# Performance work log

Hardware: AMD Instinct MI355X
Metric: run time of the kernel (lower is better)

The kernel has to match this reference:

```python
import jax, jax.numpy as jnp
import numpy as np

NSTEP, NGRID, MU = 730, 2000, 16
PRECS = 1e-5

# HBV parameter scaling ranges (parascaLst)
_LO = np.array([1, 50, 0.05, 0.01, 0.001, 0.2, 0, 0, -2.5, 0.5, 0, 0, 0.3], dtype=np.float32)
_HI = np.array([6, 1000, 0.9, 0.5, 0.2, 1, 10, 100, 2.5, 10, 0.1, 0.2, 5], dtype=np.float32)


def setup_inputs() -> dict:
    key = jax.random.key(0)
    k1, k2 = jax.random.split(key)
    u = jax.random.uniform(k1, (NSTEP, NGRID, 3), dtype=jnp.float32)
    # channel 0: precip [0,10]; channel 1: temp [-5,15]; channel 2: PET [0,5]
    scale = jnp.array([10.0, 20.0, 5.0], dtype=jnp.float32)
    shift = jnp.array([0.0, -5.0, 0.0], dtype=jnp.float32)
    x = u * scale + shift
    parameters = jax.random.uniform(k2, (NGRID, 13, MU), dtype=jnp.float32)
    return {"x": x, "parameters": parameters, "mu": MU}


def _hbv_forward(x, parameters, mu):
    Ngrid = x.shape[1]
    lo = jnp.asarray(_LO)[None, :, None]
    hi = jnp.asarray(_HI)[None, :, None]
    p = lo + parameters * (hi - lo)  # [Ngrid, 13, mu]
    (parBETA, parFC, parK0, parK1, parK2, parLP, parPERC, parUZL,
     parTT, parCFMAX, parCFR, parCWH, parBETAET) = [p[:, i, :] for i in range(13)]

    init = jnp.full((Ngrid, mu), 0.001, dtype=jnp.float32)
    state0 = (init, init, init, init, init)  # SNOWPACK, MELTWATER, SM, SUZ, SLZ

    def step(carry, inp):
        SP, MW, SM, SUZ, SLZ = carry
        Pt, Tt, Et = inp  # each [Ngrid]
        Pt, Tt, Et = Pt[:, None], Tt[:, None], Et[:, None]  # broadcast over mu
        rain = Pt * (Tt >= parTT).astype(jnp.float32)
        snow = Pt * (Tt < parTT).astype(jnp.float32)
        SP = SP + snow
        melt = jnp.minimum(jnp.maximum(parCFMAX * (Tt - parTT), 0.0), SP)
        MW = MW + melt
        SP = SP - melt
        refreezing = jnp.minimum(jnp.maximum(parCFR * parCFMAX * (parTT - Tt), 0.0), MW)
        SP = SP + refreezing
        MW = MW - refreezing
        tosoil = jnp.maximum(MW - parCWH * SP, 0.0)
        MW = MW - tosoil
        soil_wetness = jnp.clip((SM / parFC) ** parBETA, 0.0, 1.0)
        recharge = (rain + tosoil) * soil_wetness
        SM = SM + rain + tosoil - recharge
        excess = jnp.maximum(SM - parFC, 0.0)
        SM = SM - excess
        evapfactor = jnp.clip((SM / (parLP * parFC)) ** parBETAET, 0.0, 1.0)
        ETact = jnp.minimum(SM, Et * evapfactor)
        SM = jnp.maximum(SM - ETact, PRECS)
        SUZ = SUZ + recharge + excess
        PERC = jnp.minimum(SUZ, parPERC)
        SUZ = SUZ - PERC
        Q0 = parK0 * jnp.maximum(SUZ - parUZL, 0.0)
        SUZ = SUZ - Q0
        Q1 = parK1 * SUZ
        SUZ = SUZ - Q1
        SLZ = SLZ + PERC
        Q2 = parK2 * SLZ
        SLZ = SLZ - Q2
        return (SP, MW, SM, SUZ, SLZ), Q0 + Q1 + Q2

    xs = (x[:, :, 0], x[:, :, 1], x[:, :, 2])
    _, Qsimmu = jax.lax.scan(step, state0, xs)  # [Nstep, Ngrid, mu]
    Qsimave = Qsimmu.mean(-1)  # muwts=None -> mean over components
    return Qsimave[..., None]  # [Nstep, Ngrid, 1]  (routOpt=False)


def reference(x, parameters, mu):
    return _hbv_forward(x, parameters, mu)
```

## Files before the change

kernel.cpp:

```cpp
#include <hip/hip_runtime.h>

#define NSTEP  730
#define NGRID  2000
#define PRECSf 1e-5f

#define GLOBAL_AS __attribute__((address_space(1)))
#define LDS_AS    __attribute__((address_space(3)))

__device__ __forceinline__ float fast_exp2(float v) { return __builtin_amdgcn_exp2f(v); }
__device__ __forceinline__ float fast_log2(float v) { return __builtin_amdgcn_logf(v); }
__device__ __forceinline__ float med3(float a, float b, float c) {
    return __builtin_amdgcn_fmed3f(a, b, c);
}

struct Par {
    float TT, cfmax, cfmaxTT, cfrXcf, cfrTT, CWH;
    float beta, betaC, FC, betaet, betaetC;
    float PERC, omK0, k0uzl, omK1, K2;
};

#define MEMFENCE() asm volatile("" ::: "memory")
#define WAITV(N)  asm volatile("s_waitcnt vmcnt(" #N ")" ::: "memory")

template<int I>
__device__ __forceinline__ void snow1(const float4 (&xv)[16],
        float& SP, float& MW,
        float (&A)[16], float (&Ets)[16], float (&cEts)[16], const Par& c)
{
    const float Pt = xv[I].x, Tt = xv[I].y, Ex = xv[I].z;

    const float snow = (Tt < c.TT) ? Pt : 0.0f;
    const float rain = Pt - snow;
    const float mraw = fmaf(c.cfmax,   Tt, -c.cfmaxTT);
    const float rraw = fmaf(-c.cfrXcf, Tt,  c.cfrTT );
    const float SP1  = SP + snow;
    const float SP2  = med3(SP1 - mraw, 0.0f, SP1);
    const float MW1  = MW + (SP1 - SP2);
    const float MW2  = med3(MW1 - rraw, 0.0f, MW1);
    SP = SP2 + (MW1 - MW2);
    const float tosoil = fmaxf(fmaf(-c.CWH, SP, MW2), 0.0f);
    MW = MW2 - tosoil;
    A[I]    = rain + tosoil;
    Ets[I]  = Ex;
    cEts[I] = c.betaetC + fast_log2(Ex);
}

template<int I>
__device__ __forceinline__ void soil1(const float (&A)[16], const float (&Ets)[16],
        const float (&cEts)[16], float (&qbuf)[16],
        float& SM, float& SUZ, float& SLZ, const Par& c)
{
    const float Ac  = A[I];
    const float Et  = Ets[I];
    const float cEt = cEts[I];

    const float SMpA = SM + Ac;
    const float sw   = fast_exp2(fmaf(c.beta, fast_log2(SM), c.betaC));
    const float SM1  = fmaf(-Ac, sw, SMpA);
    const float SM2  = fminf(SM1, c.FC);
    const float inflow = SMpA - SM2;
    const float Ete  = fast_exp2(fmaf(c.betaet, fast_log2(SM2), cEt));
    SM = fmaxf(fmaxf(SM2 - Ete, SM2 - Et), PRECSf);

    const float SUZ1  = SUZ + inflow;
    const float PERCv = fminf(SUZ1, c.PERC);
    const float SUZ2  = SUZ1 - PERCv;
    const float SUZ3  = fminf(SUZ2, fmaf(c.omK0, SUZ2, c.k0uzl));
    const float SUZ4  = c.omK1 * SUZ3;
    SUZ = SUZ4;
    const float SLZ1 = SLZ + PERCv;
    const float Q2   = c.K2 * SLZ1;
    SLZ = SLZ1 - Q2;

    qbuf[I] = (SUZ2 - SUZ4) + Q2;
}

template<int I, int NS>
__device__ __forceinline__ void snow_pass(const float4 (&xv)[16],
        float& SP, float& MW, float (&A)[16], float (&Ets)[16], float (&cEts)[16],
        const Par& c)
{
    if constexpr (I < NS) {
        snow1<I>(xv, SP, MW, A, Ets, cEts, c);
        snow_pass<I + 1, NS>(xv, SP, MW, A, Ets, cEts, c);
    }
}

template<int I, int NS>
__device__ __forceinline__ void soil_pass(const float (&A)[16], const float (&Ets)[16],
        const float (&cEts)[16], float (&qbuf)[16],
        float& SM, float& SUZ, float& SLZ, const Par& c)
{
    if constexpr (I < NS) {
        soil1<I>(A, Ets, cEts, qbuf, SM, SUZ, SLZ, c);
        soil_pass<I + 1, NS>(A, Ets, cEts, qbuf, SM, SUZ, SLZ, c);
    }
}

template<int I, int NS>
__device__ __forceinline__ void both_pass(const float4 (&xv)[16],
        float& SP, float& MW,
        float (&An)[16], float (&Etn)[16], float (&cEtn)[16],
        const float (&Ac)[16], const float (&Etc)[16], const float (&cEtc)[16],
        float (&qbuf)[16],
        float& SM, float& SUZ, float& SLZ, const Par& c)
{
    if constexpr (I < NS) {
        soil1<I>(Ac, Etc, cEtc, qbuf, SM, SUZ, SLZ, c);
        snow1<I>(xv, SP, MW, An, Etn, cEtn, c);
        both_pass<I + 1, NS>(xv, SP, MW, An, Etn, cEtn, Ac, Etc, cEtc,
                             qbuf, SM, SUZ, SLZ, c);
    }
}

#define LOAD_XV(B)                                                             \
    _Pragma("unroll")                                                          \
    for (int i = 0; i < 16; ++i)                                               \
        xv[i] = *reinterpret_cast<const float4*>(&xs[B][i * 16 + crow * 4]);   \
    asm volatile("" :: "v"(xv[0].x),  "v"(xv[1].x),  "v"(xv[2].x),             \
                       "v"(xv[3].x),  "v"(xv[4].x),  "v"(xv[5].x),             \
                       "v"(xv[6].x),  "v"(xv[7].x),  "v"(xv[8].x),             \
                       "v"(xv[9].x),  "v"(xv[10].x), "v"(xv[11].x),            \
                       "v"(xv[12].x), "v"(xv[13].x), "v"(xv[14].x),            \
                       "v"(xv[15].x))

#define REDUCE_STORE(T0, N) do {                                               \
    float* qrow = &qt[crow * 336 + m * 20];                                    \
    *reinterpret_cast<float4*>(qrow + 0)  = make_float4(qbuf[0], qbuf[1], qbuf[2], qbuf[3]);   \
    *reinterpret_cast<float4*>(qrow + 4)  = make_float4(qbuf[4], qbuf[5], qbuf[6], qbuf[7]);   \
    *reinterpret_cast<float4*>(qrow + 8)  = make_float4(qbuf[8], qbuf[9], qbuf[10], qbuf[11]); \
    *reinterpret_cast<float4*>(qrow + 12) = make_float4(qbuf[12], qbuf[13], qbuf[14], qbuf[15]);\
    const float* qcol = &qt[crow * 336 + m];                                   \
    float s0 = qcol[0*20]  + qcol[1*20];                                       \
    float s1 = qcol[2*20]  + qcol[3*20];                                       \
    float s2 = qcol[4*20]  + qcol[5*20];                                       \
    float s3 = qcol[6*20]  + qcol[7*20];                                       \
    float s4 = qcol[8*20]  + qcol[9*20];                                       \
    float s5 = qcol[10*20] + qcol[11*20];                                      \
    float s6 = qcol[12*20] + qcol[13*20];                                      \
    float s7 = qcol[14*20] + qcol[15*20];                                      \
    s0 += s1; s2 += s3; s4 += s5; s6 += s7;                                    \
    s0 += s2; s4 += s6;                                                        \
    s0 += s4;                                                                  \
    if (m < (N)) out[(size_t)((T0) + m) * NGRID + g] = s0 * 0.0625f;           \
} while (0)

__global__ __launch_bounds__(64, 1)
void hbv_kernel(const float* __restrict__ x,
                const float* __restrict__ params,
                float* __restrict__ out)
{
    __shared__ __align__(16) float xs[2][256];
    __shared__ __align__(16) float qt[4 * 336];

    const int lane = threadIdx.x;
    const int g0   = blockIdx.x * 4;
    const int crow = lane >> 4;
    const int m    = lane & 15;
    const int g    = g0 + crow;

    const float* srcb[4];
    int ioff[4];
#pragma unroll
    for (int j = 0; j < 4; ++j) {
        const int flat = j * 64 + lane;
        const int i    = flat >> 4;
        const int cc   = (flat >> 2) & 3;
        int comp       = flat & 3; if (comp == 3) comp = 0;
        srcb[j] = x + (size_t)(g0 + cc) * 3 + comp;
        ioff[j] = i;
    }

#define ISSUE(B, T0) do {                                                      \
    MEMFENCE();                                                                \
    _Pragma("unroll")                                                          \
    for (int j = 0; j < 4; ++j) {                                              \
        int stp = (T0) + ioff[j]; stp = stp < NSTEP ? stp : NSTEP - 1;         \
        const float* s_ = srcb[j] + (size_t)stp * (NGRID * 3);                 \
        __builtin_amdgcn_global_load_lds((const GLOBAL_AS unsigned*)s_,        \
            (LDS_AS unsigned*)&xs[B][j * 64], 4, 0, 0);                        \
    }                                                                          \
    MEMFENCE();                                                                \
} while (0)

    const float lo[13] = {1.f,50.f,0.05f,0.01f,0.001f,0.2f,0.f,0.f,-2.5f,0.5f,0.f,0.f,0.3f};
    const float hi[13] = {6.f,1000.f,0.9f,0.5f,0.2f,1.f,10.f,100.f,2.5f,10.f,0.1f,0.2f,5.f};
    float p[13];
    const float* pg = params + ((size_t)g * 13) * 16 + m;
#pragma unroll
    for (int i = 0; i < 13; ++i) p[i] = lo[i] + pg[(size_t)i * 16] * (hi[i] - lo[i]);

    Par c;
    c.TT      = p[8];
    c.cfmax   = p[9];
    c.cfmaxTT = p[9] * p[8];
    c.cfrXcf  = p[10] * p[9];
    c.cfrTT   = c.cfrXcf * p[8];
    c.CWH     = p[11];
    c.beta    = p[0];
    c.betaC   = -p[0] * fast_log2(p[1]);
    c.FC      = p[1];
    c.betaet  = p[12];
    c.betaetC = -p[12] * fast_log2(p[5] * p[1]);
    c.PERC    = p[6];
    c.omK0    = 1.0f - p[2];
    c.k0uzl   = p[2] * p[7];
    c.omK1    = 1.0f - p[3];
    c.K2      = p[4];

    float SP = 0.001f, MW = 0.001f, SM = 0.001f, SUZ = 0.001f, SLZ = 0.001f;

    float4 xv[16];
    float Aa[16], EtA[16], cEtA[16];
    float Ab[16], EtB[16], cEtB[16];
    float qbuf[16];

    ISSUE(0, 0);
    ISSUE(1, 16);
    WAITV(4);
    LOAD_XV(0);
    snow_pass<0, 16>(xv, SP, MW, Aa, EtA, cEtA, c);

#define BODY_W(K, WN, AC_, ETC_, CETC_, AN_, ETN_, CETN_)                      \
    WAITV(WN);                                                                 \
    LOAD_XV(((K) + 1) & 1);                                                    \
    ISSUE((K) & 1, ((K) + 2) * 16);                                            \
    both_pass<0, 16>(xv, SP, MW, AN_, ETN_, CETN_, AC_, ETC_, CETC_,           \
                     qbuf, SM, SUZ, SLZ, c);                                   \
    REDUCE_STORE((K) * 16, 16);

    BODY_W(0, 0, Aa, EtA, cEtA, Ab, EtB, cEtB);

    for (int kk = 0; kk < 22; ++kk) {
        const int k0 = 1 + kk * 2;
        BODY_W(k0,     20, Ab, EtB, cEtB, Aa, EtA, cEtA);
        BODY_W(k0 + 1, 20, Aa, EtA, cEtA, Ab, EtB, cEtB);
    }
#undef BODY_W

    soil_pass<0, 10>(Ab, EtB, cEtB, qbuf, SM, SUZ, SLZ, c);
    REDUCE_STORE(720, 10);
#undef ISSUE
}

extern "C" void kernel_launch(void* const* d_in, const int* in_sizes, int n_in,
                              void* d_out, int out_size, void* d_ws, size_t ws_size,
                              hipStream_t stream)
{
    const float* x      = (const float*)d_in[0];
    const float* params = (const float*)d_in[1];
    float* out          = (float*)d_out;

    hipLaunchKernelGGL(hbv_kernel, dim3(500), dim3(64), 0, stream, x, params, out);
}
```

Before: 83.80 us.

## Split snow and soil recurrences across two wavefronts with LDS handoff

The single-wave kernel becomes a two-wave producer/consumer pipeline. Wave 0 loads inputs and runs the snow recurrence for the next 16-step chunk, then writes the intermediates to a double-buffered LDS array. Wave 1 runs the soil/groundwater recurrence on the previous chunk and writes per-step discharge to LDS, which wave 0 reduces and stores. The aim is to run the two serial dependency chains in parallel on separate waves, at the cost of a block barrier per chunk and extra LDS traffic. The evapotranspiration term now uses the log of SM1 instead of the clamped SM2, which changes the math whenever SM1 exceeds FC.

```diff
diff --git a/kernel.cpp b/kernel.cpp
--- a/kernel.cpp
+++ b/kernel.cpp
@@ -20,7 +20,10 @@
 };
 
 #define MEMFENCE() asm volatile("" ::: "memory")
-#define WAITV(N)  asm volatile("s_waitcnt vmcnt(" #N ")" ::: "memory")
+#define WAITV(N)   asm volatile("s_waitcnt vmcnt(" #N ")" ::: "memory")
+#define BAR() do { MEMFENCE();                                                 \
+    asm volatile("s_waitcnt lgkmcnt(0)" ::: "memory");                         \
+    __builtin_amdgcn_s_barrier(); MEMFENCE(); } while (0)
 
 template<int I>
 __device__ __forceinline__ void snow1(const float4 (&xv)[16],
@@ -59,7 +62,7 @@
     const float SM1  = fmaf(-Ac, sw, SMpA);
     const float SM2  = fminf(SM1, c.FC);
     const float inflow = SMpA - SM2;
-    const float Ete  = fast_exp2(fmaf(c.betaet, fast_log2(SM2), cEt));
+    const float Ete  = fast_exp2(fmaf(c.betaet, fast_log2(SM1), cEt));
     SM = fmaxf(fmaxf(SM2 - Ete, SM2 - Et), PRECSf);
 
     const float SUZ1  = SUZ + inflow;
@@ -97,26 +100,10 @@
     }
 }
 
-template<int I, int NS>
-__device__ __forceinline__ void both_pass(const float4 (&xv)[16],
-        float& SP, float& MW,
-        float (&An)[16], float (&Etn)[16], float (&cEtn)[16],
-        const float (&Ac)[16], const float (&Etc)[16], const float (&cEtc)[16],
-        float (&qbuf)[16],
-        float& SM, float& SUZ, float& SLZ, const Par& c)
-{
-    if constexpr (I < NS) {
-        soil1<I>(Ac, Etc, cEtc, qbuf, SM, SUZ, SLZ, c);
-        snow1<I>(xv, SP, MW, An, Etn, cEtn, c);
-        both_pass<I + 1, NS>(xv, SP, MW, An, Etn, cEtn, Ac, Etc, cEtc,
-                             qbuf, SM, SUZ, SLZ, c);
-    }
-}
-
 #define LOAD_XV(B)                                                             \
     _Pragma("unroll")                                                          \
-    for (int i = 0; i < 16; ++i)                                               \
-        xv[i] = *reinterpret_cast<const float4*>(&xs[B][i * 16 + crow * 4]);   \
+    for (int ii = 0; ii < 16; ++ii)                                            \
+        xv[ii] = *reinterpret_cast<const float4*>(&xs[B][ii * 16 + crow * 4]); \
     asm volatile("" :: "v"(xv[0].x),  "v"(xv[1].x),  "v"(xv[2].x),             \
                        "v"(xv[3].x),  "v"(xv[4].x),  "v"(xv[5].x),             \
                        "v"(xv[6].x),  "v"(xv[7].x),  "v"(xv[8].x),             \
@@ -124,13 +111,37 @@
                        "v"(xv[12].x), "v"(xv[13].x), "v"(xv[14].x),            \
                        "v"(xv[15].x))
 
-#define REDUCE_STORE(T0, N) do {                                               \
-    float* qrow = &qt[crow * 336 + m * 20];                                    \
-    *reinterpret_cast<float4*>(qrow + 0)  = make_float4(qbuf[0], qbuf[1], qbuf[2], qbuf[3]);   \
-    *reinterpret_cast<float4*>(qrow + 4)  = make_float4(qbuf[4], qbuf[5], qbuf[6], qbuf[7]);   \
-    *reinterpret_cast<float4*>(qrow + 8)  = make_float4(qbuf[8], qbuf[9], qbuf[10], qbuf[11]); \
+#define AB_WRITE(BUF)                                                          \
+    _Pragma("unroll")                                                          \
+    for (int q = 0; q < 4; ++q) {                                              \
+        ab[BUF][q    ][lane] = make_float4(A[4*q],   A[4*q+1],   A[4*q+2],   A[4*q+3]);    \
+        ab[BUF][4 + q][lane] = make_float4(Ets[4*q], Ets[4*q+1], Ets[4*q+2], Ets[4*q+3]);  \
+        ab[BUF][8 + q][lane] = make_float4(cEts[4*q],cEts[4*q+1],cEts[4*q+2],cEts[4*q+3]); \
+    }
+
+#define AB_READ(BUF) do {                                                      \
+    _Pragma("unroll")                                                          \
+    for (int j = 0; j < 12; ++j) rr[j] = ab[BUF][j][lane];                     \
+    asm volatile("" :: "v"(rr[0].x), "v"(rr[1].x), "v"(rr[2].x), "v"(rr[3].x), \
+                       "v"(rr[4].x), "v"(rr[5].x), "v"(rr[6].x), "v"(rr[7].x), \
+                       "v"(rr[8].x), "v"(rr[9].x), "v"(rr[10].x),"v"(rr[11].x));\
+    const float* rf = reinterpret_cast<const float*>(rr);                      \
+    _Pragma("unroll")                                                          \
+    for (int kk = 0; kk < 16; ++kk) {                                          \
+        Ac[kk] = rf[kk]; Etc[kk] = rf[16 + kk]; cEtc[kk] = rf[32 + kk];        \
+    }                                                                          \
+} while (0)
+
+#define QT_WRITE(BUF) do {                                                     \
+    float* qrow = &qt[BUF][crow * 336 + m * 20];                               \
+    *reinterpret_cast<float4*>(qrow + 0)  = make_float4(qbuf[0], qbuf[1], qbuf[2], qbuf[3]);    \
+    *reinterpret_cast<float4*>(qrow + 4)  = make_float4(qbuf[4], qbuf[5], qbuf[6], qbuf[7]);    \
+    *reinterpret_cast<float4*>(qrow + 8)  = make_float4(qbuf[8], qbuf[9], qbuf[10], qbuf[11]);  \
     *reinterpret_cast<float4*>(qrow + 12) = make_float4(qbuf[12], qbuf[13], qbuf[14], qbuf[15]);\
-    const float* qcol = &qt[crow * 336 + m];                                   \
+} while (0)
+
+#define REDUCE_OUT(BUF, T0, N) do {                                            \
+    const float* qcol = &qt[BUF][crow * 336 + m];                              \
     float s0 = qcol[0*20]  + qcol[1*20];                                       \
     float s1 = qcol[2*20]  + qcol[3*20];                                       \
     float s2 = qcol[4*20]  + qcol[5*20];                                       \
@@ -140,20 +151,22 @@
     float s6 = qcol[12*20] + qcol[13*20];                                      \
     float s7 = qcol[14*20] + qcol[15*20];                                      \
     s0 += s1; s2 += s3; s4 += s5; s6 += s7;                                    \
-    s0 += s2; s4 += s6;                                                        \
-    s0 += s4;                                                                  \
+    s0 += s2; s4 += s6; s0 += s4;                                              \
     if (m < (N)) out[(size_t)((T0) + m) * NGRID + g] = s0 * 0.0625f;           \
 } while (0)
 
-__global__ __launch_bounds__(64, 1)
+__global__ __launch_bounds__(128, 1)
 void hbv_kernel(const float* __restrict__ x,
                 const float* __restrict__ params,
                 float* __restrict__ out)
 {
-    __shared__ __align__(16) float xs[2][256];
-    __shared__ __align__(16) float qt[4 * 336];
-
-    const int lane = threadIdx.x;
+    __shared__ __align__(16) float4 ab[2][12][64];
+    __shared__ __align__(16) float  xs[2][256];
+    __shared__ __align__(16) float  qt[2][4 * 336];
+
+    const int tid  = threadIdx.x;
+    const int wid  = tid >> 6;
+    const int lane = tid & 63;
     const int g0   = blockIdx.x * 4;
     const int crow = lane >> 4;
     const int m    = lane & 15;
@@ -211,35 +224,42 @@
     float SP = 0.001f, MW = 0.001f, SM = 0.001f, SUZ = 0.001f, SLZ = 0.001f;
 
     float4 xv[16];
-    float Aa[16], EtA[16], cEtA[16];
-    float Ab[16], EtB[16], cEtB[16];
-    float qbuf[16];
-
-    ISSUE(0, 0);
-    ISSUE(1, 16);
-    WAITV(4);
-    LOAD_XV(0);
-    snow_pass<0, 16>(xv, SP, MW, Aa, EtA, cEtA, c);
-
-#define BODY_W(K, WN, AC_, ETC_, CETC_, AN_, ETN_, CETN_)                      \
-    WAITV(WN);                                                                 \
-    LOAD_XV(((K) + 1) & 1);                                                    \
-    ISSUE((K) & 1, ((K) + 2) * 16);                                            \
-    both_pass<0, 16>(xv, SP, MW, AN_, ETN_, CETN_, AC_, ETC_, CETC_,           \
-                     qbuf, SM, SUZ, SLZ, c);                                   \
-    REDUCE_STORE((K) * 16, 16);
-
-    BODY_W(0, 0, Aa, EtA, cEtA, Ab, EtB, cEtB);
-
-    for (int kk = 0; kk < 22; ++kk) {
-        const int k0 = 1 + kk * 2;
-        BODY_W(k0,     20, Ab, EtB, cEtB, Aa, EtA, cEtA);
-        BODY_W(k0 + 1, 20, Aa, EtA, cEtA, Ab, EtB, cEtB);
-    }
-#undef BODY_W
-
-    soil_pass<0, 10>(Ab, EtB, cEtB, qbuf, SM, SUZ, SLZ, c);
-    REDUCE_STORE(720, 10);
+    float  A[16], Ets[16], cEts[16];
+    float4 rr[12];
+    float  Ac[16], Etc[16], cEtc[16];
+    float  qbuf[16];
+
+    if (wid == 0) {
+        ISSUE(0, 0);
+        ISSUE(1, 16);
+        WAITV(4);
+        LOAD_XV(0);
+        snow_pass<0, 16>(xv, SP, MW, A, Ets, cEts, c);
+        AB_WRITE(0);
+    }
+    BAR();
+
+    for (int i = 0; i < 46; ++i) {
+        if (wid == 0) {
+            if (i <= 43) ISSUE(i & 1, (i + 2) * 16);
+            if (i <= 44) {
+                if (i == 44)      { WAITV(16); }
+                else if (i >= 2)  { WAITV(20); }
+                else              { WAITV(4);  }
+                LOAD_XV((i + 1) & 1);
+                snow_pass<0, 16>(xv, SP, MW, A, Ets, cEts, c);
+                AB_WRITE((i + 1) & 1);
+            }
+            if (i >= 1) REDUCE_OUT((i - 1) & 1, (i - 1) * 16, 16);
+        } else {
+            AB_READ(i & 1);
+            if (i < 45) soil_pass<0, 16>(Ac, Etc, cEtc, qbuf, SM, SUZ, SLZ, c);
+            else        soil_pass<0, 10>(Ac, Etc, cEtc, qbuf, SM, SUZ, SLZ, c);
+            QT_WRITE(i & 1);
+        }
+        BAR();
+    }
+    if (wid == 0) REDUCE_OUT(1, 720, 10);
 #undef ISSUE
 }
 
@@ -251,5 +271,5 @@
     const float* params = (const float*)d_in[1];
     float* out          = (float*)d_out;
 
-    hipLaunchKernelGGL(hbv_kernel, dim3(500), dim3(64), 0, stream, x, params, out);
-}
+    hipLaunchKernelGGL(hbv_kernel, dim3(500), dim3(128), 0, stream, x, params, out);
+}
```

Measured after the change: 91.77 us. 9.5% more time.

## Process two mu components per lane and eight grid cells per wavefront

Applied to the files above, without the earlier changes.

Each lane now carries two independent HBV state chains (mu j and j+8), so a wavefront covers eight grid cells and the launch halves to 250 blocks. The two interleaved recurrences give the scheduler independent work to hide the latency of the serial per-step dependency chain. The staging buffers, load issue pattern and LDS reduction are resized for the new mapping, and the evapotranspiration power now uses SM1 instead of the clamped SM2, which can change results when soil moisture exceeds FC. Fewer wavefronts run than there are compute units, and register pressure roughly doubles.

```diff
diff --git a/kernel.cpp b/kernel.cpp
--- a/kernel.cpp
+++ b/kernel.cpp
@@ -22,13 +22,9 @@
 #define MEMFENCE() asm volatile("" ::: "memory")
 #define WAITV(N)  asm volatile("s_waitcnt vmcnt(" #N ")" ::: "memory")
 
-template<int I>
-__device__ __forceinline__ void snow1(const float4 (&xv)[16],
-        float& SP, float& MW,
-        float (&A)[16], float (&Ets)[16], float (&cEts)[16], const Par& c)
-{
-    const float Pt = xv[I].x, Tt = xv[I].y, Ex = xv[I].z;
-
+__device__ __forceinline__ float snow_core(float Pt, float Tt,
+        float& SP, float& MW, const Par& c)
+{
     const float snow = (Tt < c.TT) ? Pt : 0.0f;
     const float rain = Pt - snow;
     const float mraw = fmaf(c.cfmax,   Tt, -c.cfmaxTT);
@@ -40,26 +36,18 @@
     SP = SP2 + (MW1 - MW2);
     const float tosoil = fmaxf(fmaf(-c.CWH, SP, MW2), 0.0f);
     MW = MW2 - tosoil;
-    A[I]    = rain + tosoil;
-    Ets[I]  = Ex;
-    cEts[I] = c.betaetC + fast_log2(Ex);
-}
-
-template<int I>
-__device__ __forceinline__ void soil1(const float (&A)[16], const float (&Ets)[16],
-        const float (&cEts)[16], float (&qbuf)[16],
+    return rain + tosoil;
+}
+
+__device__ __forceinline__ float soil_core(float Ac, float Et, float cEt,
         float& SM, float& SUZ, float& SLZ, const Par& c)
 {
-    const float Ac  = A[I];
-    const float Et  = Ets[I];
-    const float cEt = cEts[I];
-
     const float SMpA = SM + Ac;
     const float sw   = fast_exp2(fmaf(c.beta, fast_log2(SM), c.betaC));
     const float SM1  = fmaf(-Ac, sw, SMpA);
     const float SM2  = fminf(SM1, c.FC);
     const float inflow = SMpA - SM2;
-    const float Ete  = fast_exp2(fmaf(c.betaet, fast_log2(SM2), cEt));
+    const float Ete  = fast_exp2(fmaf(c.betaet, fast_log2(SM1), cEt));
     SM = fmaxf(fmaxf(SM2 - Ete, SM2 - Et), PRECSf);
 
     const float SUZ1  = SUZ + inflow;
@@ -71,52 +59,90 @@
     const float SLZ1 = SLZ + PERCv;
     const float Q2   = c.K2 * SLZ1;
     SLZ = SLZ1 - Q2;
-
-    qbuf[I] = (SUZ2 - SUZ4) + Q2;
+    return (SUZ2 - SUZ4) + Q2;
+}
+
+template<int I>
+__device__ __forceinline__ void snow1(const float4 (&xv)[16],
+        float& SP0, float& MW0, float& SP1, float& MW1,
+        float (&A0)[16], float (&A1)[16], float (&Ets)[16],
+        float (&cE0)[16], float (&cE1)[16],
+        const Par& c0, const Par& c1)
+{
+    const float Pt = xv[I].x, Tt = xv[I].y, Ex = xv[I].z;
+    const float lEx = fast_log2(Ex);
+    Ets[I] = Ex;
+    A0[I] = snow_core(Pt, Tt, SP0, MW0, c0);
+    cE0[I] = c0.betaetC + lEx;
+    A1[I] = snow_core(Pt, Tt, SP1, MW1, c1);
+    cE1[I] = c1.betaetC + lEx;
+}
+
+template<int I>
+__device__ __forceinline__ void soil1(const float (&A0)[16], const float (&A1)[16],
+        const float (&Ets)[16], const float (&cE0)[16], const float (&cE1)[16],
+        float (&qbuf)[16],
+        float& SM0, float& SUZ0, float& SLZ0,
+        float& SM1, float& SUZ1, float& SLZ1,
+        const Par& c0, const Par& c1)
+{
+    const float q0 = soil_core(A0[I], Ets[I], cE0[I], SM0, SUZ0, SLZ0, c0);
+    const float q1 = soil_core(A1[I], Ets[I], cE1[I], SM1, SUZ1, SLZ1, c1);
+    qbuf[I] = q0 + q1;
 }
 
 template<int I, int NS>
 __device__ __forceinline__ void snow_pass(const float4 (&xv)[16],
-        float& SP, float& MW, float (&A)[16], float (&Ets)[16], float (&cEts)[16],
-        const Par& c)
+        float& SP0, float& MW0, float& SP1, float& MW1,
+        float (&A0)[16], float (&A1)[16], float (&Ets)[16],
+        float (&cE0)[16], float (&cE1)[16], const Par& c0, const Par& c1)
 {
     if constexpr (I < NS) {
-        snow1<I>(xv, SP, MW, A, Ets, cEts, c);
-        snow_pass<I + 1, NS>(xv, SP, MW, A, Ets, cEts, c);
+        snow1<I>(xv, SP0, MW0, SP1, MW1, A0, A1, Ets, cE0, cE1, c0, c1);
+        snow_pass<I + 1, NS>(xv, SP0, MW0, SP1, MW1, A0, A1, Ets, cE0, cE1, c0, c1);
     }
 }
 
 template<int I, int NS>
-__device__ __forceinline__ void soil_pass(const float (&A)[16], const float (&Ets)[16],
-        const float (&cEts)[16], float (&qbuf)[16],
-        float& SM, float& SUZ, float& SLZ, const Par& c)
+__device__ __forceinline__ void soil_pass(const float (&A0)[16], const float (&A1)[16],
+        const float (&Ets)[16], const float (&cE0)[16], const float (&cE1)[16],
+        float (&qbuf)[16],
+        float& SM0, float& SUZ0, float& SLZ0,
+        float& SM1, float& SUZ1, float& SLZ1,
+        const Par& c0, const Par& c1)
 {
     if constexpr (I < NS) {
-        soil1<I>(A, Ets, cEts, qbuf, SM, SUZ, SLZ, c);
-        soil_pass<I + 1, NS>(A, Ets, cEts, qbuf, SM, SUZ, SLZ, c);
+        soil1<I>(A0, A1, Ets, cE0, cE1, qbuf, SM0, SUZ0, SLZ0, SM1, SUZ1, SLZ1, c0, c1);
+        soil_pass<I + 1, NS>(A0, A1, Ets, cE0, cE1, qbuf,
+                             SM0, SUZ0, SLZ0, SM1, SUZ1, SLZ1, c0, c1);
     }
 }
 
 template<int I, int NS>
 __device__ __forceinline__ void both_pass(const float4 (&xv)[16],
-        float& SP, float& MW,
-        float (&An)[16], float (&Etn)[16], float (&cEtn)[16],
-        const float (&Ac)[16], const float (&Etc)[16], const float (&cEtc)[16],
+        float& SP0, float& MW0, float& SP1, float& MW1,
+        float (&An0)[16], float (&An1)[16], float (&Etn)[16],
+        float (&cEn0)[16], float (&cEn1)[16],
+        const float (&Ac0)[16], const float (&Ac1)[16], const float (&Etc)[16],
+        const float (&cEc0)[16], const float (&cEc1)[16],
         float (&qbuf)[16],
-        float& SM, float& SUZ, float& SLZ, const Par& c)
+        float& SM0, float& SUZ0, float& SLZ0,
+        float& SM1, float& SUZ1, float& SLZ1,
+        const Par& c0, const Par& c1)
 {
     if constexpr (I < NS) {
-        soil1<I>(Ac, Etc, cEtc, qbuf, SM, SUZ, SLZ, c);
-        snow1<I>(xv, SP, MW, An, Etn, cEtn, c);
-        both_pass<I + 1, NS>(xv, SP, MW, An, Etn, cEtn, Ac, Etc, cEtc,
-                             qbuf, SM, SUZ, SLZ, c);
+        soil1<I>(Ac0, Ac1, Etc, cEc0, cEc1, qbuf, SM0, SUZ0, SLZ0, SM1, SUZ1, SLZ1, c0, c1);
+        snow1<I>(xv, SP0, MW0, SP1, MW1, An0, An1, Etn, cEn0, cEn1, c0, c1);
+        both_pass<I + 1, NS>(xv, SP0, MW0, SP1, MW1, An0, An1, Etn, cEn0, cEn1,
+                             Ac0, Ac1, Etc, cEc0, cEc1, qbuf,
+                             SM0, SUZ0, SLZ0, SM1, SUZ1, SLZ1, c0, c1);
     }
 }
 
 #define LOAD_XV(B)                                                             \
     _Pragma("unroll")                                                          \
-    for (int i = 0; i < 16; ++i)                                               \
-        xv[i] = *reinterpret_cast<const float4*>(&xs[B][i * 16 + crow * 4]);   \
+    for (int ii = 0; ii < 16; ++ii)                                            \
+        xv[ii] = *reinterpret_cast<const float4*>(&xs[B][ii * 32 + cc * 4]);   \
     asm volatile("" :: "v"(xv[0].x),  "v"(xv[1].x),  "v"(xv[2].x),             \
                        "v"(xv[3].x),  "v"(xv[4].x),  "v"(xv[5].x),             \
                        "v"(xv[6].x),  "v"(xv[7].x),  "v"(xv[8].x),             \
@@ -125,24 +151,25 @@
                        "v"(xv[15].x))
 
 #define REDUCE_STORE(T0, N) do {                                               \
-    float* qrow = &qt[crow * 336 + m * 20];                                    \
-    *reinterpret_cast<float4*>(qrow + 0)  = make_float4(qbuf[0], qbuf[1], qbuf[2], qbuf[3]);   \
-    *reinterpret_cast<float4*>(qrow + 4)  = make_float4(qbuf[4], qbuf[5], qbuf[6], qbuf[7]);   \
-    *reinterpret_cast<float4*>(qrow + 8)  = make_float4(qbuf[8], qbuf[9], qbuf[10], qbuf[11]); \
+    float* qrow = &qt[cc * 168 + j2 * 20];                                     \
+    *reinterpret_cast<float4*>(qrow + 0)  = make_float4(qbuf[0], qbuf[1], qbuf[2], qbuf[3]);    \
+    *reinterpret_cast<float4*>(qrow + 4)  = make_float4(qbuf[4], qbuf[5], qbuf[6], qbuf[7]);    \
+    *reinterpret_cast<float4*>(qrow + 8)  = make_float4(qbuf[8], qbuf[9], qbuf[10], qbuf[11]);  \
     *reinterpret_cast<float4*>(qrow + 12) = make_float4(qbuf[12], qbuf[13], qbuf[14], qbuf[15]);\
-    const float* qcol = &qt[crow * 336 + m];                                   \
-    float s0 = qcol[0*20]  + qcol[1*20];                                       \
-    float s1 = qcol[2*20]  + qcol[3*20];                                       \
-    float s2 = qcol[4*20]  + qcol[5*20];                                       \
-    float s3 = qcol[6*20]  + qcol[7*20];                                       \
-    float s4 = qcol[8*20]  + qcol[9*20];                                       \
-    float s5 = qcol[10*20] + qcol[11*20];                                      \
-    float s6 = qcol[12*20] + qcol[13*20];                                      \
-    float s7 = qcol[14*20] + qcol[15*20];                                      \
-    s0 += s1; s2 += s3; s4 += s5; s6 += s7;                                    \
-    s0 += s2; s4 += s6;                                                        \
-    s0 += s4;                                                                  \
-    if (m < (N)) out[(size_t)((T0) + m) * NGRID + g] = s0 * 0.0625f;           \
+    const float* qc1 = &qt[cc * 168 + j2];                                     \
+    float a0 = qc1[0*20] + qc1[1*20];                                          \
+    float a1 = qc1[2*20] + qc1[3*20];                                          \
+    float a2 = qc1[4*20] + qc1[5*20];                                          \
+    float a3 = qc1[6*20] + qc1[7*20];                                          \
+    a0 += a1; a2 += a3; a0 += a2;                                              \
+    out[(size_t)((T0) + j2) * NGRID + g] = a0 * 0.0625f;                       \
+    const float* qc2 = &qt[cc * 168 + 8 + j2];                                 \
+    float b0 = qc2[0*20] + qc2[1*20];                                          \
+    float b1 = qc2[2*20] + qc2[3*20];                                          \
+    float b2 = qc2[4*20] + qc2[5*20];                                          \
+    float b3 = qc2[6*20] + qc2[7*20];                                          \
+    b0 += b1; b2 += b3; b0 += b2;                                              \
+    if (8 + j2 < (N)) out[(size_t)((T0) + 8 + j2) * NGRID + g] = b0 * 0.0625f; \
 } while (0)
 
 __global__ __launch_bounds__(64, 1)
@@ -150,31 +177,31 @@
                 const float* __restrict__ params,
                 float* __restrict__ out)
 {
-    __shared__ __align__(16) float xs[2][256];
-    __shared__ __align__(16) float qt[4 * 336];
+    __shared__ __align__(16) float xs[2][512];
+    __shared__ __align__(16) float qt[8 * 168];
 
     const int lane = threadIdx.x;
-    const int g0   = blockIdx.x * 4;
-    const int crow = lane >> 4;
-    const int m    = lane & 15;
-    const int g    = g0 + crow;
-
-    const float* srcb[4];
-    int ioff[4];
+    const int g0   = blockIdx.x * 8;
+    const int cc   = lane >> 3;
+    const int j2   = lane & 7;
+    const int g    = g0 + cc;
+
+    const float* srcb[8];
+    int ioff[8];
 #pragma unroll
-    for (int j = 0; j < 4; ++j) {
+    for (int j = 0; j < 8; ++j) {
         const int flat = j * 64 + lane;
-        const int i    = flat >> 4;
-        const int cc   = (flat >> 2) & 3;
+        const int i    = flat >> 5;
+        const int ce   = (flat >> 2) & 7;
         int comp       = flat & 3; if (comp == 3) comp = 0;
-        srcb[j] = x + (size_t)(g0 + cc) * 3 + comp;
+        srcb[j] = x + (size_t)(g0 + ce) * 3 + comp;
         ioff[j] = i;
     }
 
 #define ISSUE(B, T0) do {                                                      \
     MEMFENCE();                                                                \
     _Pragma("unroll")                                                          \
-    for (int j = 0; j < 4; ++j) {                                              \
+    for (int j = 0; j < 8; ++j) {                                              \
         int stp = (T0) + ioff[j]; stp = stp < NSTEP ? stp : NSTEP - 1;         \
         const float* s_ = srcb[j] + (size_t)stp * (NGRID * 3);                 \
         __builtin_amdgcn_global_load_lds((const GLOBAL_AS unsigned*)s_,        \
@@ -185,60 +212,71 @@
 
     const float lo[13] = {1.f,50.f,0.05f,0.01f,0.001f,0.2f,0.f,0.f,-2.5f,0.5f,0.f,0.f,0.3f};
     const float hi[13] = {6.f,1000.f,0.9f,0.5f,0.2f,1.f,10.f,100.f,2.5f,10.f,0.1f,0.2f,5.f};
-    float p[13];
-    const float* pg = params + ((size_t)g * 13) * 16 + m;
+    float p0[13], p1[13];
+    const float* pg = params + ((size_t)g * 13) * 16;
 #pragma unroll
-    for (int i = 0; i < 13; ++i) p[i] = lo[i] + pg[(size_t)i * 16] * (hi[i] - lo[i]);
-
-    Par c;
-    c.TT      = p[8];
-    c.cfmax   = p[9];
-    c.cfmaxTT = p[9] * p[8];
-    c.cfrXcf  = p[10] * p[9];
-    c.cfrTT   = c.cfrXcf * p[8];
-    c.CWH     = p[11];
-    c.beta    = p[0];
-    c.betaC   = -p[0] * fast_log2(p[1]);
-    c.FC      = p[1];
-    c.betaet  = p[12];
-    c.betaetC = -p[12] * fast_log2(p[5] * p[1]);
-    c.PERC    = p[6];
-    c.omK0    = 1.0f - p[2];
-    c.k0uzl   = p[2] * p[7];
-    c.omK1    = 1.0f - p[3];
+    for (int i = 0; i < 13; ++i) {
+        p0[i] = lo[i] + pg[(size_t)i * 16 + j2    ] * (hi[i] - lo[i]);
+        p1[i] = lo[i] + pg[(size_t)i * 16 + j2 + 8] * (hi[i] - lo[i]);
+    }
+
+#define MKPAR(c, p)                                                            \
+    c.TT      = p[8];                                                          \
+    c.cfmax   = p[9];                                                          \
+    c.cfmaxTT = p[9] * p[8];                                                   \
+    c.cfrXcf  = p[10] * p[9];                                                  \
+    c.cfrTT   = c.cfrXcf * p[8];                                               \
+    c.CWH     = p[11];                                                         \
+    c.beta    = p[0];                                                          \
+    c.betaC   = -p[0] * fast_log2(p[1]);                                       \
+    c.FC      = p[1];                                                          \
+    c.betaet  = p[12];                                                         \
+    c.betaetC = -p[12] * fast_log2(p[5] * p[1]);                               \
+    c.PERC    = p[6];                                                          \
+    c.omK0    = 1.0f - p[2];                                                   \
+    c.k0uzl   = p[2] * p[7];                                                   \
+    c.omK1    = 1.0f - p[3];                                                   \
     c.K2      = p[4];
 
-    float SP = 0.001f, MW = 0.001f, SM = 0.001f, SUZ = 0.001f, SLZ = 0.001f;
+    Par c0, c1;
+    MKPAR(c0, p0);
+    MKPAR(c1, p1);
+#undef MKPAR
+
+    float SP0 = 0.001f, MW0 = 0.001f, SM0 = 0.001f, SUZ0 = 0.001f, SLZ0 = 0.001f;
+    float SP1 = 0.001f, MW1 = 0.001f, SM1 = 0.001f, SUZ1 = 0.001f, SLZ1 = 0.001f;
 
     float4 xv[16];
-    float Aa[16], EtA[16], cEtA[16];
-    float Ab[16], EtB[16], cEtB[16];
+    float A0a[16], A1a[16], Eta[16], cE0a[16], cE1a[16];
+    float A0b[16], A1b[16], Etb[16], cE0b[16], cE1b[16];
     float qbuf[16];
 
     ISSUE(0, 0);
     ISSUE(1, 16);
-    WAITV(4);
+    WAITV(8);
     LOAD_XV(0);
-    snow_pass<0, 16>(xv, SP, MW, Aa, EtA, cEtA, c);
-
-#define BODY_W(K, WN, AC_, ETC_, CETC_, AN_, ETN_, CETN_)                      \
+    snow_pass<0, 16>(xv, SP0, MW0, SP1, MW1, A0a, A1a, Eta, cE0a, cE1a, c0, c1);
+
+#define BODY_W(K, WN, AC0,AC1,ETC,CEC0,CEC1, AN0,AN1,ETN,CEN0,CEN1)            \
     WAITV(WN);                                                                 \
     LOAD_XV(((K) + 1) & 1);                                                    \
     ISSUE((K) & 1, ((K) + 2) * 16);                                            \
-    both_pass<0, 16>(xv, SP, MW, AN_, ETN_, CETN_, AC_, ETC_, CETC_,           \
-                     qbuf, SM, SUZ, SLZ, c);                                   \
+    both_pass<0, 16>(xv, SP0, MW0, SP1, MW1, AN0, AN1, ETN, CEN0, CEN1,        \
+                     AC0, AC1, ETC, CEC0, CEC1, qbuf,                          \
+                     SM0, SUZ0, SLZ0, SM1, SUZ1, SLZ1, c0, c1);                \
     REDUCE_STORE((K) * 16, 16);
 
-    BODY_W(0, 0, Aa, EtA, cEtA, Ab, EtB, cEtB);
+    BODY_W(0, 0, A0a,A1a,Eta,cE0a,cE1a, A0b,A1b,Etb,cE0b,cE1b);
 
     for (int kk = 0; kk < 22; ++kk) {
         const int k0 = 1 + kk * 2;
-        BODY_W(k0,     20, Ab, EtB, cEtB, Aa, EtA, cEtA);
-        BODY_W(k0 + 1, 20, Aa, EtA, cEtA, Ab, EtB, cEtB);
+        BODY_W(k0,     2, A0b,A1b,Etb,cE0b,cE1b, A0a,A1a,Eta,cE0a,cE1a);
+        BODY_W(k0 + 1, 2, A0a,A1a,Eta,cE0a,cE1a, A0b,A1b,Etb,cE0b,cE1b);
     }
 #undef BODY_W
 
-    soil_pass<0, 10>(Ab, EtB, cEtB, qbuf, SM, SUZ, SLZ, c);
+    soil_pass<0, 10>(A0b, A1b, Etb, cE0b, cE1b, qbuf,
+                     SM0, SUZ0, SLZ0, SM1, SUZ1, SLZ1, c0, c1);
     REDUCE_STORE(720, 10);
 #undef ISSUE
 }
@@ -251,5 +289,5 @@
     const float* params = (const float*)d_in[1];
     float* out          = (float*)d_out;
 
-    hipLaunchKernelGGL(hbv_kernel, dim3(500), dim3(64), 0, stream, x, params, out);
-}
+    hipLaunchKernelGGL(hbv_kernel, dim3(250), dim3(64), 0, stream, x, params, out);
+}
```

Result: slower. 143.1 us (+70.8%).

## Software-pipeline routing one step behind soil update and drop precomputed log of PET

Applied to the files above, without the earlier changes.

Restructures the per-step recurrence so the groundwater routing of step I-1 is interleaved with the soil update of step I, which shortens the serial dependency chain through SM. It also interleaves the snow computation with the soil math. The evaporation term is now computed as Et*exp2(...) instead of adding log2(Et) inside the exponent, which removes one log per step and the cEt arrays. The vmcnt wait threshold changes from 20 to 16. The risks are slightly different rounding and higher register pressure from the extra live values.

```diff
diff --git a/kernel.cpp b/kernel.cpp
--- a/kernel.cpp
+++ b/kernel.cpp
@@ -22,47 +22,10 @@
 #define MEMFENCE() asm volatile("" ::: "memory")
 #define WAITV(N)  asm volatile("s_waitcnt vmcnt(" #N ")" ::: "memory")
 
-template<int I>
-__device__ __forceinline__ void snow1(const float4 (&xv)[16],
-        float& SP, float& MW,
-        float (&A)[16], float (&Ets)[16], float (&cEts)[16], const Par& c)
-{
-    const float Pt = xv[I].x, Tt = xv[I].y, Ex = xv[I].z;
-
-    const float snow = (Tt < c.TT) ? Pt : 0.0f;
-    const float rain = Pt - snow;
-    const float mraw = fmaf(c.cfmax,   Tt, -c.cfmaxTT);
-    const float rraw = fmaf(-c.cfrXcf, Tt,  c.cfrTT );
-    const float SP1  = SP + snow;
-    const float SP2  = med3(SP1 - mraw, 0.0f, SP1);
-    const float MW1  = MW + (SP1 - SP2);
-    const float MW2  = med3(MW1 - rraw, 0.0f, MW1);
-    SP = SP2 + (MW1 - MW2);
-    const float tosoil = fmaxf(fmaf(-c.CWH, SP, MW2), 0.0f);
-    MW = MW2 - tosoil;
-    A[I]    = rain + tosoil;
-    Ets[I]  = Ex;
-    cEts[I] = c.betaetC + fast_log2(Ex);
-}
-
-template<int I>
-__device__ __forceinline__ void soil1(const float (&A)[16], const float (&Ets)[16],
-        const float (&cEts)[16], float (&qbuf)[16],
-        float& SM, float& SUZ, float& SLZ, const Par& c)
-{
-    const float Ac  = A[I];
-    const float Et  = Ets[I];
-    const float cEt = cEts[I];
-
-    const float SMpA = SM + Ac;
-    const float sw   = fast_exp2(fmaf(c.beta, fast_log2(SM), c.betaC));
-    const float SM1  = fmaf(-Ac, sw, SMpA);
-    const float SM2  = fminf(SM1, c.FC);
-    const float inflow = SMpA - SM2;
-    const float Ete  = fast_exp2(fmaf(c.betaet, fast_log2(SM2), cEt));
-    SM = fmaxf(fmaxf(SM2 - Ete, SM2 - Et), PRECSf);
-
-    const float SUZ1  = SUZ + inflow;
+__device__ __forceinline__ float route_step(float infl,
+        float& SUZ, float& SLZ, const Par& c)
+{
+    const float SUZ1  = SUZ + infl;
     const float PERCv = fminf(SUZ1, c.PERC);
     const float SUZ2  = SUZ1 - PERCv;
     const float SUZ3  = fminf(SUZ2, fmaf(c.omK0, SUZ2, c.k0uzl));
@@ -71,52 +34,93 @@
     const float SLZ1 = SLZ + PERCv;
     const float Q2   = c.K2 * SLZ1;
     SLZ = SLZ1 - Q2;
-
-    qbuf[I] = (SUZ2 - SUZ4) + Q2;
+    return (SUZ2 - SUZ4) + Q2;
+}
+
+template<int I, bool SNOW>
+__device__ __forceinline__ void step1(const float4 (&xv)[16],
+        const float (&A)[16], const float (&Ets)[16],
+        float (&An)[16], float (&Etn)[16],
+        float (&qbuf)[16], float& infl,
+        float& SM, float& SUZ, float& SLZ,
+        float& SP, float& MW, const Par& c)
+{
+    const float Ac   = A[I];
+    const float Et   = Ets[I];
+    const float SMpA = SM + Ac;
+    const float lg   = fast_log2(SM);
+    float rain = 0.0f, SP2v = 0.0f, MW1v = 0.0f, rrawv = 0.0f, Ex = 0.0f;
+    if constexpr (SNOW) {
+        const float Pt = xv[I].x, Tt = xv[I].y;
+        Ex = xv[I].z;
+        const float snow = (Tt < c.TT) ? Pt : 0.0f;
+        rain = Pt - snow;
+        const float mraw = fmaf(c.cfmax, Tt, -c.cfmaxTT);
+        rrawv = fmaf(-c.cfrXcf, Tt, c.cfrTT);
+        const float SP1 = SP + snow;
+        SP2v = med3(SP1 - mraw, 0.0f, SP1);
+        MW1v = MW + (SP1 - SP2v);
+    }
+    const float sw = fast_exp2(fmaf(c.beta, lg, c.betaC));
+    if constexpr (I >= 1) qbuf[I - 1] = route_step(infl, SUZ, SLZ, c);
+    const float SM1 = fmaf(-Ac, sw, SMpA);
+    const float lg1 = fast_log2(SM1);
+    if constexpr (SNOW) {
+        const float MW2 = med3(MW1v - rrawv, 0.0f, MW1v);
+        SP = SP2v + (MW1v - MW2);
+        const float tosoil = fmaxf(fmaf(-c.CWH, SP, MW2), 0.0f);
+        MW = MW2 - tosoil;
+        An[I]  = rain + tosoil;
+        Etn[I] = Ex;
+    }
+    const float SM2 = fminf(SM1, c.FC);
+    infl = SMpA - SM2;
+    const float Ete = Et * fast_exp2(fmaf(c.betaet, lg1, c.betaetC));
+    SM = fmaxf(fmaxf(SM2 - Ete, SM2 - Et), PRECSf);
+}
+
+template<int I, int NS, bool SNOW>
+__device__ __forceinline__ void steps_pass(const float4 (&xv)[16],
+        const float (&A)[16], const float (&Ets)[16],
+        float (&An)[16], float (&Etn)[16],
+        float (&qbuf)[16], float& infl,
+        float& SM, float& SUZ, float& SLZ,
+        float& SP, float& MW, const Par& c)
+{
+    if constexpr (I < NS) {
+        step1<I, SNOW>(xv, A, Ets, An, Etn, qbuf, infl, SM, SUZ, SLZ, SP, MW, c);
+        steps_pass<I + 1, NS, SNOW>(xv, A, Ets, An, Etn, qbuf, infl,
+                                    SM, SUZ, SLZ, SP, MW, c);
+    }
 }
 
 template<int I, int NS>
 __device__ __forceinline__ void snow_pass(const float4 (&xv)[16],
-        float& SP, float& MW, float (&A)[16], float (&Ets)[16], float (&cEts)[16],
-        const Par& c)
+        float& SP, float& MW, float (&A)[16], float (&Ets)[16], const Par& c)
 {
     if constexpr (I < NS) {
-        snow1<I>(xv, SP, MW, A, Ets, cEts, c);
-        snow_pass<I + 1, NS>(xv, SP, MW, A, Ets, cEts, c);
-    }
-}
-
-template<int I, int NS>
-__device__ __forceinline__ void soil_pass(const float (&A)[16], const float (&Ets)[16],
-        const float (&cEts)[16], float (&qbuf)[16],
-        float& SM, float& SUZ, float& SLZ, const Par& c)
-{
-    if constexpr (I < NS) {
-        soil1<I>(A, Ets, cEts, qbuf, SM, SUZ, SLZ, c);
-        soil_pass<I + 1, NS>(A, Ets, cEts, qbuf, SM, SUZ, SLZ, c);
-    }
-}
-
-template<int I, int NS>
-__device__ __forceinline__ void both_pass(const float4 (&xv)[16],
-        float& SP, float& MW,
-        float (&An)[16], float (&Etn)[16], float (&cEtn)[16],
-        const float (&Ac)[16], const float (&Etc)[16], const float (&cEtc)[16],
-        float (&qbuf)[16],
-        float& SM, float& SUZ, float& SLZ, const Par& c)
-{
-    if constexpr (I < NS) {
-        soil1<I>(Ac, Etc, cEtc, qbuf, SM, SUZ, SLZ, c);
-        snow1<I>(xv, SP, MW, An, Etn, cEtn, c);
-        both_pass<I + 1, NS>(xv, SP, MW, An, Etn, cEtn, Ac, Etc, cEtc,
-                             qbuf, SM, SUZ, SLZ, c);
+        const float Pt = xv[I].x, Tt = xv[I].y, Ex = xv[I].z;
+        const float snow = (Tt < c.TT) ? Pt : 0.0f;
+        const float rain = Pt - snow;
+        const float mraw = fmaf(c.cfmax, Tt, -c.cfmaxTT);
+        const float rraw = fmaf(-c.cfrXcf, Tt, c.cfrTT);
+        const float SP1  = SP + snow;
+        const float SP2  = med3(SP1 - mraw, 0.0f, SP1);
+        const float MW1  = MW + (SP1 - SP2);
+        const float MW2  = med3(MW1 - rraw, 0.0f, MW1);
+        SP = SP2 + (MW1 - MW2);
+        const float tosoil = fmaxf(fmaf(-c.CWH, SP, MW2), 0.0f);
+        MW = MW2 - tosoil;
+        A[I]   = rain + tosoil;
+        Ets[I] = Ex;
+        snow_pass<I + 1, NS>(xv, SP, MW, A, Ets, c);
     }
 }
 
 #define LOAD_XV(B)                                                             \
     _Pragma("unroll")                                                          \
-    for (int i = 0; i < 16; ++i)                                               \
-        xv[i] = *reinterpret_cast<const float4*>(&xs[B][i * 16 + crow * 4]);   \
+    for (int ii = 0; ii < 16; ++ii)                                            \
+        xv[ii] = *reinterpret_cast<const float4*>(&xs[B][ii * 16 + crow * 4]); \
     asm volatile("" :: "v"(xv[0].x),  "v"(xv[1].x),  "v"(xv[2].x),             \
                        "v"(xv[3].x),  "v"(xv[4].x),  "v"(xv[5].x),             \
                        "v"(xv[6].x),  "v"(xv[7].x),  "v"(xv[8].x),             \
@@ -126,9 +130,9 @@
 
 #define REDUCE_STORE(T0, N) do {                                               \
     float* qrow = &qt[crow * 336 + m * 20];                                    \
-    *reinterpret_cast<float4*>(qrow + 0)  = make_float4(qbuf[0], qbuf[1], qbuf[2], qbuf[3]);   \
-    *reinterpret_cast<float4*>(qrow + 4)  = make_float4(qbuf[4], qbuf[5], qbuf[6], qbuf[7]);   \
-    *reinterpret_cast<float4*>(qrow + 8)  = make_float4(qbuf[8], qbuf[9], qbuf[10], qbuf[11]); \
+    *reinterpret_cast<float4*>(qrow + 0)  = make_float4(qbuf[0], qbuf[1], qbuf[2], qbuf[3]);    \
+    *reinterpret_cast<float4*>(qrow + 4)  = make_float4(qbuf[4], qbuf[5], qbuf[6], qbuf[7]);    \
+    *reinterpret_cast<float4*>(qrow + 8)  = make_float4(qbuf[8], qbuf[9], qbuf[10], qbuf[11]);  \
     *reinterpret_cast<float4*>(qrow + 12) = make_float4(qbuf[12], qbuf[13], qbuf[14], qbuf[15]);\
     const float* qcol = &qt[crow * 336 + m];                                   \
     float s0 = qcol[0*20]  + qcol[1*20];                                       \
@@ -140,8 +144,7 @@
     float s6 = qcol[12*20] + qcol[13*20];                                      \
     float s7 = qcol[14*20] + qcol[15*20];                                      \
     s0 += s1; s2 += s3; s4 += s5; s6 += s7;                                    \
-    s0 += s2; s4 += s6;                                                        \
-    s0 += s4;                                                                  \
+    s0 += s2; s4 += s6; s0 += s4;                                              \
     if (m < (N)) out[(size_t)((T0) + m) * NGRID + g] = s0 * 0.0625f;           \
 } while (0)
 
@@ -211,34 +214,38 @@
     float SP = 0.001f, MW = 0.001f, SM = 0.001f, SUZ = 0.001f, SLZ = 0.001f;
 
     float4 xv[16];
-    float Aa[16], EtA[16], cEtA[16];
-    float Ab[16], EtB[16], cEtB[16];
+    float Aa[16], Eta[16];
+    float Ab[16], Etb[16];
     float qbuf[16];
+    float infl = 0.0f;
 
     ISSUE(0, 0);
     ISSUE(1, 16);
     WAITV(4);
     LOAD_XV(0);
-    snow_pass<0, 16>(xv, SP, MW, Aa, EtA, cEtA, c);
-
-#define BODY_W(K, WN, AC_, ETC_, CETC_, AN_, ETN_, CETN_)                      \
+    snow_pass<0, 16>(xv, SP, MW, Aa, Eta, c);
+
+#define BODY_W(K, WN, AC_, ETC_, AN_, ETN_)                                    \
     WAITV(WN);                                                                 \
     LOAD_XV(((K) + 1) & 1);                                                    \
     ISSUE((K) & 1, ((K) + 2) * 16);                                            \
-    both_pass<0, 16>(xv, SP, MW, AN_, ETN_, CETN_, AC_, ETC_, CETC_,           \
-                     qbuf, SM, SUZ, SLZ, c);                                   \
+    steps_pass<0, 16, true>(xv, AC_, ETC_, AN_, ETN_, qbuf, infl,              \
+                            SM, SUZ, SLZ, SP, MW, c);                          \
+    qbuf[15] = route_step(infl, SUZ, SLZ, c);                                  \
     REDUCE_STORE((K) * 16, 16);
 
-    BODY_W(0, 0, Aa, EtA, cEtA, Ab, EtB, cEtB);
+    BODY_W(0, 0, Aa, Eta, Ab, Etb);
 
     for (int kk = 0; kk < 22; ++kk) {
         const int k0 = 1 + kk * 2;
-        BODY_W(k0,     20, Ab, EtB, cEtB, Aa, EtA, cEtA);
-        BODY_W(k0 + 1, 20, Aa, EtA, cEtA, Ab, EtB, cEtB);
+        BODY_W(k0,     16, Ab, Etb, Aa, Eta);
+        BODY_W(k0 + 1, 16, Aa, Eta, Ab, Etb);
     }
 #undef BODY_W
 
-    soil_pass<0, 10>(Ab, EtB, cEtB, qbuf, SM, SUZ, SLZ, c);
+    steps_pass<0, 10, false>(xv, Ab, Etb, Aa, Eta, qbuf, infl,
+                             SM, SUZ, SLZ, SP, MW, c);
+    qbuf[9] = route_step(infl, SUZ, SLZ, c);
     REDUCE_STORE(720, 10);
 #undef ISSUE
 }
```

Result: faster. 80.15 us (median of 2 runs) (-4.4%).
